# Kernel optimization log

Measured on AMD Instinct MI355X. Metric: run time of the kernel, lower is better.

The kernel has to match this reference:

```python
import jax, jax.numpy as jnp
import numpy as np

EPS = 1e-5

def conv2d(x, w, stride=1, padding=1, dilation=1):
    # x: [N, C, H, W], w: [O, I, kh, kw]
    return jax.lax.conv_general_dilated(
        x, w, (stride, stride), [(padding, padding), (padding, padding)],
        rhs_dilation=(dilation, dilation),
        dimension_numbers=('NCHW', 'OIHW', 'NCHW'))


def setup_inputs() -> dict:
    key = jax.random.key(0)
    ks = jax.random.split(key, 7)
    T, N, Cin, H, W = 16, 4, 64, 64, 64
    Cout = 64
    x = jax.random.normal(ks[0], (T, N, Cin, H, W), dtype=jnp.float32)
    gamma = jnp.ones((Cin,), jnp.float32)
    beta = jnp.zeros((Cin,), jnp.float32)
    conv1_w = jax.random.normal(ks[1], (3 * Cout, Cin, 3, 3), jnp.float32) * 0.02
    conv1_b = jax.random.normal(ks[2], (3 * Cout,), jnp.float32) * 0.02
    w_h2h = jax.random.normal(ks[3], (3 * Cout, Cout, 3, 3), jnp.float32) * 0.02
    w_c2h = jax.random.normal(ks[4], (3 * Cout, Cout, 3, 3), jnp.float32) * 0.02
    return {"x": x, "gamma": gamma, "beta": beta, "conv1_w": conv1_w,
            "conv1_b": conv1_b, "w_h2h": w_h2h, "w_c2h": w_c2h}


def reference(x, gamma, beta, conv1_w, conv1_b, w_h2h, w_c2h):
    T, N, Cin, H, W = x.shape
    Cout = w_h2h.shape[1]
    # time_to_batch: [T, N, C, H, W] -> [T*N, C, H, W]
    xb = x.reshape(T * N, Cin, H, W)
    # BatchNorm2d (training mode: biased batch stats over N*T, H, W)
    mean = jnp.mean(xb, axis=(0, 2, 3), keepdims=True)
    var = jnp.var(xb, axis=(0, 2, 3), keepdims=True)
    g = gamma.reshape(1, Cin, 1, 1)
    b = beta.reshape(1, Cin, 1, 1)
    bnx = (xb - mean) * jax.lax.rsqrt(var + EPS) * g + b
    # conv1: Cin -> 3*Cout
    y = conv2d(bnx, conv1_w, stride=1, padding=1) + conv1_b.reshape(1, -1, 1, 1)
    # batch_to_time: -> [T, N, 3*Cout, H, W]
    y = y.reshape(T, N, 3 * Cout, H, W)

    # ConvLSTMCell: zero init state is exact (h2h/c2h convs have no bias)
    h0 = jnp.zeros((N, Cout, H, W), y.dtype)
    c0 = jnp.zeros((N, Cout, H, W), y.dtype)

    def step(carry, yt):
        h, c = carry
        tmp = conv2d(c, w_c2h, padding=1) + conv2d(h, w_h2h, padding=1) + yt
        cc_f, cc_o, cc_g = jnp.split(tmp, 3, axis=1)
        f = jax.nn.sigmoid(cc_f)
        o = jax.nn.sigmoid(cc_o)
        gg = jnp.tanh(cc_g)
        c_new = f * c + (1.0 - f) * gg
        h_new = o * jnp.tanh(c_new)
        return (h_new, c_new), h_new

    _, hs = jax.lax.scan(step, (h0, c0), y)
    return hs  # [T, N, Cout, H, W]
```

## Files before the change

kernel.cpp:

```cpp
#include <hip/hip_runtime.h>

typedef unsigned short u16;
typedef unsigned int   u32;
typedef __attribute__((ext_vector_type(8))) short short8;
typedef __attribute__((ext_vector_type(4))) float f32x4;

typedef __attribute__((address_space(1))) const void GASV;
typedef __attribute__((address_space(3))) void LASV;

#define IMG_BYTES  557568
#define WS_SCALE   0
#define WS_SHIFT   256
#define WS_PART    512
#define WS_WA      8704
#define WS_BNXP    672256
#define WS_HC      (WS_BNXP + 64*IMG_BYTES)
#define WS_CSTATE  (WS_HC + 16*IMG_BYTES)

__device__ __forceinline__ u16 f2b(float f){
  u32 x = __float_as_uint(f);
  return (u16)((x + 0x7fffu + ((x>>16)&1u)) >> 16);
}
__device__ __forceinline__ float sigm(float x){ return 1.f/(1.f+__expf(-x)); }
__device__ __forceinline__ float tanh_(float x){
  float e = __expf(2.f*fabsf(x));
  float t = 1.f - 2.f/(e+1.f);
  return copysignf(t, x);
}

__global__ void k_wt(const float* __restrict__ c1, const float* __restrict__ c2h,
                     const float* __restrict__ h2h, u16* __restrict__ wA){
  int idx = blockIdx.x*256 + threadIdx.x;
  int e = idx & 7;
  int lane = (idx >> 3) & 63;
  int v = idx >> 9;
  int f2 = v % 12;  v /= 12;
  int oh = v & 1;
  int stage = v >> 1;
  int cc = f2 / 6, gate = (f2 % 6) >> 1, og2 = f2 & 1;
  int j = stage / 9, tap = stage % 9;
  int och = gate*64 + (oh*2 + og2)*16 + (lane & 15);
  int c = cc*32 + (lane >> 4)*8 + e;
  const float* src = (j==0) ? c1 : ((j==1) ? c2h : h2h);
  wA[idx] = f2b(src[(och*64 + c)*9 + tap]);
}

__global__ void k_bnsum(const float* __restrict__ x, float* __restrict__ part){
  int c = blockIdx.x & 63, g = blockIdx.x >> 6;
  int tid = threadIdx.x, w = tid >> 6, lane = tid & 63;
  float s = 0.f, s2 = 0.f;
  for (int im = 0; im < 4; ++im){
    const float* base = x + (((size_t)((g*4+im)*64 + c)) << 12);
    #pragma unroll
    for (int it = 0; it < 4; ++it){
      float4 v = *(const float4*)(base + (((it<<8) + tid) << 2));
      s  += v.x + v.y + v.z + v.w;
      s2 += v.x*v.x + v.y*v.y + v.z*v.z + v.w*v.w;
    }
  }
  #pragma unroll
  for (int off = 32; off > 0; off >>= 1){
    s  += __shfl_down(s,  off);
    s2 += __shfl_down(s2, off);
  }
  __shared__ float red[8];
  if (lane == 0){ red[w] = s; red[4+w] = s2; }
  __syncthreads();
  if (tid == 0){
    float S  = red[0]+red[1]+red[2]+red[3];
    float S2 = red[4]+red[5]+red[6]+red[7];
    part[(g<<7) + c] = S;
    part[(g<<7) + 64 + c] = S2;
  }
}

__global__ void k_bnfin(const float* __restrict__ part, const float* __restrict__ gamma,
                        const float* __restrict__ beta, float* __restrict__ scale,
                        float* __restrict__ shift){
  int c = threadIdx.x;
  float S = 0.f, S2 = 0.f;
  for (int g = 0; g < 16; ++g){ S += part[(g<<7)+c]; S2 += part[(g<<7)+64+c]; }
  const float inv = 1.f/262144.f;
  float mean = S*inv;
  float var  = S2*inv - mean*mean;
  float sc = gamma[c] * rsqrtf(var + 1e-5f);
  scale[c] = sc;
  shift[c] = beta[c] - mean*sc;
}

__global__ void k_bnx(const float* __restrict__ x, const float* __restrict__ scale,
                      const float* __restrict__ shift, char* __restrict__ bnxp){
  int img = blockIdx.x / 66, rp = blockIdx.x % 66;
  int tid = threadIdx.x;
  char* dstrow = bnxp + (size_t)img*IMG_BYTES + (size_t)rp*8448;
  const uint4 z = {0,0,0,0};
  if (rp == 0 || rp == 65){
    for (int i = tid; i < 528; i += 256) ((uint4*)dstrow)[i] = z;
    return;
  }
  if (tid < 16)
    *(uint4*)(dstrow + (tid>>3)*(65*128) + (tid&7)*16) = z;
  int r = rp - 1;
  int col = tid & 63, cq = tid >> 6;
  const float* xb = x + (((size_t)(img*64 + cq*16)) << 12) + (r<<6) + col;
  union { u16 u[16]; uint4 v[2]; } pk;
  #pragma unroll
  for (int i = 0; i < 16; ++i){
    int c = cq*16 + i;
    float vv = xb[((size_t)i) << 12];
    pk.u[i] = f2b(vv*scale[c] + shift[c]);
  }
  char* dst = dstrow + (size_t)(col + 1)*128 + cq*32;
  *(uint4*)dst = pk.v[0];
  *(uint4*)(dst+16) = pk.v[1];
}

#define SM_RING(b) (28512 + (b)*12288)

#define STAGE_W(s, b) do {                                                      \
  const char* _gs = wA + ((size_t)((s)*2 + oh))*12288 + (w*3)*1024 + lane*16;   \
  char* _ls = smem + SM_RING(b) + (w*3)*1024;                                   \
  __builtin_amdgcn_global_load_lds((GASV*)(_gs),        (LASV*)(_ls),        16, 0, 0); \
  __builtin_amdgcn_global_load_lds((GASV*)(_gs + 1024), (LASV*)(_ls + 1024), 16, 0, 0); \
  __builtin_amdgcn_global_load_lds((GASV*)(_gs + 2048), (LASV*)(_ls + 2048), 16, 0, 0); \
} while(0)

#define WAIT3_BAR() do {                                                        \
  asm volatile("s_waitcnt vmcnt(3)\n\ts_barrier" ::: "memory");                 \
  __builtin_amdgcn_sched_barrier(0);                                            \
} while(0)
#define WAIT0_BAR() do {                                                        \
  asm volatile("s_waitcnt vmcnt(0)\n\ts_barrier" ::: "memory");                 \
  __builtin_amdgcn_sched_barrier(0);                                            \
} while(0)

__global__ __launch_bounds__(256, 2) void k_step(
    const char* __restrict__ bnxp,
    const char* __restrict__ cpad_s, const char* __restrict__ hpad_s,
    char* __restrict__ cpad_d, char* __restrict__ hpad_d,
    const char* __restrict__ wA, const float* __restrict__ b1,
    float* __restrict__ cstate, float* __restrict__ out, int t)
{
  __shared__ __align__(16) char smem[65376];
  const int tid = threadIdx.x;
  const int w = tid >> 6, lane = tid & 63;
  const int l15 = lane & 15, l4 = lane >> 4;
  const int og2 = w >> 1, ch = w & 1;
  const int bid = blockIdx.x;
  const int oh = bid & 1, row = (bid >> 1) & 63, n = bid >> 7;

  const char* gb0 = bnxp   + (size_t)(t*4+n)*IMG_BYTES + row*8448;
  const char* gb1 = cpad_s + (size_t)n*IMG_BYTES + row*8448;
  const char* gb2 = hpad_s + (size_t)n*IMG_BYTES + row*8448;

  f32x4 acc[3][2];
  #pragma unroll
  for (int a = 0; a < 3; ++a)
    #pragma unroll
    for (int b = 0; b < 2; ++b)
      acc[a][b] = (f32x4){0.f,0.f,0.f,0.f};

  STAGE_W(0, 0);
  STAGE_W(1, 1);

  #pragma unroll
  for (int j = 0; j < 3; ++j){
    const char* gbj = (j==0) ? gb0 : ((j==1) ? gb1 : gb2);
    for (int i = tid; i < 1584; i += 256){
      int rr = i / 528, iw = i % 528;
      *(uint4*)(smem + rr*9504 + (iw>>3)*144 + (iw&7)*16) =
          *(const uint4*)(gbj + rr*8448 + iw*16);
    }
    __syncthreads();

    #pragma unroll
    for (int tap = 0; tap < 9; ++tap){
      const int s = j*9 + tap;
      if (s < 25) STAGE_W(s+2, (s+2)%3);
      {
        const int kh = tap/3, kw = tap%3;
        const char* ab0 = smem + SM_RING(s%3) + og2*1024 + lane*16;
        const char* ib0 = smem + kh*9504 + ((ch<<5) + kw + l15)*144 + l4*16;
        #pragma unroll
        for (int cc = 0; cc < 2; ++cc){
          short8 af = *(const short8*)(ab0 + cc*6144);
          short8 ao = *(const short8*)(ab0 + cc*6144 + 2048);
          short8 ag = *(const short8*)(ab0 + cc*6144 + 4096);
          #pragma unroll
          for (int cf = 0; cf < 2; ++cf){
            short8 bf = *(const short8*)(ib0 + cc*64 + cf*2304);
            acc[0][cf] = __builtin_amdgcn_mfma_f32_16x16x32_bf16(af, bf, acc[0][cf], 0,0,0);
            acc[1][cf] = __builtin_amdgcn_mfma_f32_16x16x32_bf16(ao, bf, acc[1][cf], 0,0,0);
            acc[2][cf] = __builtin_amdgcn_mfma_f32_16x16x32_bf16(ag, bf, acc[2][cf], 0,0,0);
          }
        }
      }
      if (s < 26){
        if (s == 25) WAIT0_BAR();
        else         WAIT3_BAR();
      }
    }
  }

  const size_t cb = ((size_t)(n*64)) << 12;
  const size_t ob = ((size_t)((t*4+n)*64)) << 12;
  const int gc0 = ((oh<<1) + og2)*16 + l4*4;
  char* hrow = hpad_d + (size_t)n*IMG_BYTES + (size_t)(row+1)*8448;
  char* crow = cpad_d + (size_t)n*IMG_BYTES + (size_t)(row+1)*8448;

  #pragma unroll
  for (int cf = 0; cf < 2; ++cf){
    const int col = (ch<<5) + (cf<<4) + l15;
    const int p = (row<<6) + col;
    union { u16 u[4]; uint2 v; } hp, cp2;
    #pragma unroll
    for (int reg = 0; reg < 4; ++reg){
      const int gc = gc0 + reg;
      float fv = acc[0][cf][reg] + b1[gc];
      float ov = acc[1][cf][reg] + b1[64+gc];
      float gv = acc[2][cf][reg] + b1[128+gc];
      float f  = sigm(fv);
      float og_ = sigm(ov);
      float g  = tanh_(gv);
      float* cptr = cstate + cb + (((size_t)gc)<<12) + p;
      float cprev = *cptr;
      float cn = f*cprev + (1.f-f)*g;
      float hn = og_ * tanh_(cn);
      *cptr = cn;
      out[ob + (((size_t)gc)<<12) + p] = hn;
      hp.u[reg]  = f2b(hn);
      cp2.u[reg] = f2b(cn);
    }
    *(uint2*)(hrow + (size_t)(col+1)*128 + gc0*2) = hp.v;
    *(uint2*)(crow + (size_t)(col+1)*128 + gc0*2) = cp2.v;
  }
}

extern "C" void kernel_launch(void* const* d_in, const int* in_sizes, int n_in,
                              void* d_out, int out_size, void* d_ws, size_t ws_size,
                              hipStream_t stream)
{
  (void)in_sizes; (void)n_in; (void)out_size; (void)ws_size;
  const float* x     = (const float*)d_in[0];
  const float* gamma = (const float*)d_in[1];
  const float* beta  = (const float*)d_in[2];
  const float* c1w   = (const float*)d_in[3];
  const float* c1b   = (const float*)d_in[4];
  const float* wh2h  = (const float*)d_in[5];
  const float* wc2h  = (const float*)d_in[6];
  char* ws  = (char*)d_ws;
  float* out = (float*)d_out;

  char* hpad0 = ws + WS_HC;
  char* cpad0 = ws + WS_HC + (size_t)4*IMG_BYTES;
  char* hpad1 = ws + WS_HC + (size_t)8*IMG_BYTES;
  char* cpad1 = ws + WS_HC + (size_t)12*IMG_BYTES;

  hipMemsetAsync(ws + WS_HC, 0, (size_t)16*IMG_BYTES, stream);
  hipMemsetAsync(ws + WS_CSTATE, 0, (size_t)4*64*4096*4, stream);

  k_wt<<<1296, 256, 0, stream>>>(c1w, wc2h, wh2h, (u16*)(ws + WS_WA));
  k_bnsum<<<1024, 256, 0, stream>>>(x, (float*)(ws + WS_PART));
  k_bnfin<<<1, 64, 0, stream>>>((const float*)(ws + WS_PART), gamma, beta,
                                (float*)(ws + WS_SCALE), (float*)(ws + WS_SHIFT));
  k_bnx<<<4224, 256, 0, stream>>>(x, (const float*)(ws + WS_SCALE),
                                  (const float*)(ws + WS_SHIFT), ws + WS_BNXP);
  for (int t = 0; t < 16; ++t){
    const char* cs = (t & 1) ? cpad1 : cpad0;
    const char* hs = (t & 1) ? hpad1 : hpad0;
    char* cd = (t & 1) ? cpad0 : cpad1;
    char* hd = (t & 1) ? hpad0 : hpad1;
    k_step<<<512, 256, 0, stream>>>(ws + WS_BNXP, cs, hs, cd, hd,
                                    ws + WS_WA, c1b,
                                    (float*)(ws + WS_CSTATE), out, t);
  }
}
```

Baseline: 391.6 us.

## Process two output rows per block to share staged weights across waves

Result: faster. 372.5 us (-4.9%).

```diff
diff --git a/kernel.cpp b/kernel.cpp
--- a/kernel.cpp
+++ b/kernel.cpp
@@ -16,6 +16,9 @@
 #define WS_BNXP    672256
 #define WS_HC      (WS_BNXP + 64*IMG_BYTES)
 #define WS_CSTATE  (WS_HC + 16*IMG_BYTES)
+
+#define SM_RING_OFF 38016
+#define SMEM_TOT    (38016 + 4*12288)
 
 __device__ __forceinline__ u16 f2b(float f){
   u32 x = __float_as_uint(f);
@@ -115,43 +118,43 @@
   *(uint4*)(dst+16) = pk.v[1];
 }
 
-#define SM_RING(b) (28512 + (b)*12288)
-
-#define STAGE_W(s, b) do {                                                      \
-  const char* _gs = wA + ((size_t)((s)*2 + oh))*12288 + (w*3)*1024 + lane*16;   \
-  char* _ls = smem + SM_RING(b) + (w*3)*1024;                                   \
-  __builtin_amdgcn_global_load_lds((GASV*)(_gs),        (LASV*)(_ls),        16, 0, 0); \
-  __builtin_amdgcn_global_load_lds((GASV*)(_gs + 1024), (LASV*)(_ls + 1024), 16, 0, 0); \
-  __builtin_amdgcn_global_load_lds((GASV*)(_gs + 2048), (LASV*)(_ls + 2048), 16, 0, 0); \
+#define STAGE_W(v) do {                                                         \
+  if (w < 4){                                                                   \
+    int _vj = jp + (v)/9; if (_vj >= 3) _vj -= 3;                               \
+    int _vt = tp + (v)%9; if (_vt >= 9) _vt -= 9;                               \
+    const char* _gs = wA + ((size_t)((_vj*9 + _vt)*2 + oh))*12288               \
+                        + w*3072 + lane*16;                                     \
+    char* _ls = smem + SM_RING_OFF + ((v)&3)*12288 + w*3072;                    \
+    __builtin_amdgcn_global_load_lds((GASV*)(_gs),        (LASV*)(_ls),        16, 0, 0); \
+    __builtin_amdgcn_global_load_lds((GASV*)(_gs + 1024), (LASV*)(_ls + 1024), 16, 0, 0); \
+    __builtin_amdgcn_global_load_lds((GASV*)(_gs + 2048), (LASV*)(_ls + 2048), 16, 0, 0); \
+  }                                                                             \
 } while(0)
 
-#define WAIT3_BAR() do {                                                        \
-  asm volatile("s_waitcnt vmcnt(3)\n\ts_barrier" ::: "memory");                 \
+#define WAITN_BAR(N) do {                                                       \
+  asm volatile("s_waitcnt vmcnt(" #N ")\n\ts_barrier" ::: "memory");            \
   __builtin_amdgcn_sched_barrier(0);                                            \
 } while(0)
-#define WAIT0_BAR() do {                                                        \
-  asm volatile("s_waitcnt vmcnt(0)\n\ts_barrier" ::: "memory");                 \
-  __builtin_amdgcn_sched_barrier(0);                                            \
-} while(0)
-
-__global__ __launch_bounds__(256, 2) void k_step(
+
+__global__ __launch_bounds__(512, 1) void k_step(
     const char* __restrict__ bnxp,
     const char* __restrict__ cpad_s, const char* __restrict__ hpad_s,
     char* __restrict__ cpad_d, char* __restrict__ hpad_d,
     const char* __restrict__ wA, const float* __restrict__ b1,
     float* __restrict__ cstate, float* __restrict__ out, int t)
 {
-  __shared__ __align__(16) char smem[65376];
+  extern __shared__ __align__(16) char smem[];
   const int tid = threadIdx.x;
   const int w = tid >> 6, lane = tid & 63;
   const int l15 = lane & 15, l4 = lane >> 4;
-  const int og2 = w >> 1, ch = w & 1;
+  const int wr = w >> 2, og2 = (w >> 1) & 1, ch = w & 1;
   const int bid = blockIdx.x;
-  const int oh = bid & 1, row = (bid >> 1) & 63, n = bid >> 7;
-
-  const char* gb0 = bnxp   + (size_t)(t*4+n)*IMG_BYTES + row*8448;
-  const char* gb1 = cpad_s + (size_t)n*IMG_BYTES + row*8448;
-  const char* gb2 = hpad_s + (size_t)n*IMG_BYTES + row*8448;
+  const int oh = bid & 1, rp = (bid >> 1) & 31, n = bid >> 6;
+  const int jp = bid % 3, tp = bid % 9;
+
+  const char* gb0 = bnxp   + (size_t)(t*4+n)*IMG_BYTES + rp*16896;
+  const char* gb1 = cpad_s + (size_t)n*IMG_BYTES + rp*16896;
+  const char* gb2 = hpad_s + (size_t)n*IMG_BYTES + rp*16896;
 
   f32x4 acc[3][2];
   #pragma unroll
@@ -160,13 +163,13 @@
     for (int b = 0; b < 2; ++b)
       acc[a][b] = (f32x4){0.f,0.f,0.f,0.f};
 
-  STAGE_W(0, 0);
-  STAGE_W(1, 1);
-
-  #pragma unroll
-  for (int j = 0; j < 3; ++j){
-    const char* gbj = (j==0) ? gb0 : ((j==1) ? gb1 : gb2);
-    for (int i = tid; i < 1584; i += 256){
+  STAGE_W(0); STAGE_W(1); STAGE_W(2);
+
+  #pragma unroll
+  for (int jj = 0; jj < 3; ++jj){
+    int jv = jp + jj; if (jv >= 3) jv -= 3;
+    const char* gbj = (jv==0) ? gb0 : ((jv==1) ? gb1 : gb2);
+    for (int i = tid; i < 2112; i += 512){
       int rr = i / 528, iw = i % 528;
       *(uint4*)(smem + rr*9504 + (iw>>3)*144 + (iw&7)*16) =
           *(const uint4*)(gbj + rr*8448 + iw*16);
@@ -174,13 +177,14 @@
     __syncthreads();
 
     #pragma unroll
-    for (int tap = 0; tap < 9; ++tap){
-      const int s = j*9 + tap;
-      if (s < 25) STAGE_W(s+2, (s+2)%3);
+    for (int tt = 0; tt < 9; ++tt){
+      const int u = jj*9 + tt;
+      if (u <= 23) STAGE_W(u+3);
       {
-        const int kh = tap/3, kw = tap%3;
-        const char* ab0 = smem + SM_RING(s%3) + og2*1024 + lane*16;
-        const char* ib0 = smem + kh*9504 + ((ch<<5) + kw + l15)*144 + l4*16;
+        int tv = tp + tt; if (tv >= 9) tv -= 9;
+        const int kh = tv/3, kw = tv - kh*3;
+        const char* ab0 = smem + SM_RING_OFF + (u&3)*12288 + og2*1024 + lane*16;
+        const char* ib0 = smem + (wr + kh)*9504 + ((ch<<5) + kw + l15)*144 + l4*16;
         #pragma unroll
         for (int cc = 0; cc < 2; ++cc){
           short8 af = *(const short8*)(ab0 + cc*6144);
@@ -195,23 +199,23 @@
           }
         }
       }
-      if (s < 26){
-        if (s == 25) WAIT0_BAR();
-        else         WAIT3_BAR();
-      }
-    }
-  }
-
+      if (u <= 23)      WAITN_BAR(6);
+      else if (u == 24) WAITN_BAR(3);
+      else if (u == 25) WAITN_BAR(0);
+    }
+  }
+
+  const int r = (rp << 1) + wr;
   const size_t cb = ((size_t)(n*64)) << 12;
   const size_t ob = ((size_t)((t*4+n)*64)) << 12;
   const int gc0 = ((oh<<1) + og2)*16 + l4*4;
-  char* hrow = hpad_d + (size_t)n*IMG_BYTES + (size_t)(row+1)*8448;
-  char* crow = cpad_d + (size_t)n*IMG_BYTES + (size_t)(row+1)*8448;
+  char* hrow = hpad_d + (size_t)n*IMG_BYTES + (size_t)(r+1)*8448;
+  char* crow = cpad_d + (size_t)n*IMG_BYTES + (size_t)(r+1)*8448;
 
   #pragma unroll
   for (int cf = 0; cf < 2; ++cf){
     const int col = (ch<<5) + (cf<<4) + l15;
-    const int p = (row<<6) + col;
+    const int p = (r<<6) + col;
     union { u16 u[4]; uint2 v; } hp, cp2;
     #pragma unroll
     for (int reg = 0; reg < 4; ++reg){
@@ -251,6 +255,9 @@
   char* ws  = (char*)d_ws;
   float* out = (float*)d_out;
 
+  hipFuncSetAttribute(reinterpret_cast<const void*>(k_step),
+                      hipFuncAttributeMaxDynamicSharedMemorySize, SMEM_TOT);
+
   char* hpad0 = ws + WS_HC;
   char* cpad0 = ws + WS_HC + (size_t)4*IMG_BYTES;
   char* hpad1 = ws + WS_HC + (size_t)8*IMG_BYTES;
@@ -270,8 +277,8 @@
     const char* hs = (t & 1) ? hpad1 : hpad0;
     char* cd = (t & 1) ? cpad0 : cpad1;
     char* hd = (t & 1) ? hpad0 : hpad1;
-    k_step<<<512, 256, 0, stream>>>(ws + WS_BNXP, cs, hs, cd, hd,
-                                    ws + WS_WA, c1b,
-                                    (float*)(ws + WS_CSTATE), out, t);
-  }
-}
+    k_step<<<256, 512, SMEM_TOT, stream>>>(ws + WS_BNXP, cs, hs, cd, hd,
+                                           ws + WS_WA, c1b,
+                                           (float*)(ws + WS_CSTATE), out, t);
+  }
+}
```
